# Kernel tuning notes

Hardware: AMD Instinct MI355X
Metric: run time of the kernel (lower is better)

## Reference

```python
import math
import jax, jax.numpy as jnp
import numpy as np

N_STEPS = 4
D_ENERGY = 128
FEATURE_DIM = 1024
B, N = 4, 2048


def setup_inputs() -> dict:
    key = jax.random.key(0)
    ks = jax.random.split(key, 5)
    scale = 1.0 / math.sqrt(FEATURE_DIM)
    return {
        "features": jax.random.normal(ks[0], (B, N, FEATURE_DIM), dtype=jnp.float32),
        "W_q": jax.random.normal(ks[1], (FEATURE_DIM, D_ENERGY), dtype=jnp.float32) * scale,
        "W_k": jax.random.normal(ks[2], (FEATURE_DIM, D_ENERGY), dtype=jnp.float32) * scale,
        "charge_w": jax.random.normal(ks[3], (FEATURE_DIM, 1), dtype=jnp.float32) * scale,
        "charge_b": jnp.zeros((1,), dtype=jnp.float32),
        "locality_scale": jnp.float32(1.0),
        "step_size": jnp.float32(0.5),
        "charge_decay": jnp.float32(0.3),
    }


def reference(features, W_q, W_k, charge_w, charge_b, locality_scale, step_size, charge_decay):
    Bn, Nn, _ = features.shape
    # compatibility: [B,N,N]
    Q = jnp.einsum("bnf,fe->bne", features, W_q)
    K = jnp.einsum("bnf,fe->bne", features, W_k)
    compat = jnp.einsum("bqe,bke->bqk", Q, K) / jnp.sqrt(jnp.float32(D_ENERGY))
    # locality bias: locality_scale / max(|i-j|, 1)
    pos = jnp.arange(Nn, dtype=jnp.float32)
    dist = jnp.maximum(jnp.abs(pos[None, :] - pos[:, None]), 1.0)
    locality = locality_scale / dist  # [N,N]
    # initial charge in (0,1): [B,N]
    charge = jax.nn.sigmoid(jnp.einsum("bnf,fo->bno", features, charge_w)[..., 0] + charge_b[0])
    base = compat + locality[None]  # [B,N,N], fixed across steps
    logits = base
    for _ in range(N_STEPS):
        attn = jax.nn.softmax(logits, axis=-1)
        received = attn.sum(axis=-2)  # [B,N] column sums
        charge = charge * (1.0 - charge_decay * jax.nn.sigmoid(received - 1.0))
        energy = -base * charge[..., :, None] * charge[..., None, :]
        logits = logits - step_size * energy
    return jax.nn.softmax(logits, axis=-1)
```

## Files before the change

kernel.cpp:

```cpp
#include <hip/hip_runtime.h>
#include <math.h>

namespace {
constexpr int NB = 4;
constexpr int NN = 2048;
constexpr int FD = 1024;
constexpr int DE = 128;
constexpr int BN = NB * NN;

constexpr size_t BASE_OFF  = 0;
constexpr size_t PARTQ_OFF = 0;
constexpr size_t PARTK_OFF = 4194304;
constexpr size_t FH_OFF    = 8388608;
constexpr size_t FL_OFF    = 12582912;
constexpr size_t QKHL_OFF  = 16777216;
constexpr size_t C_OFF     = QKHL_OFF + 2097152;
constexpr size_t R_OFF     = C_OFF + 5 * (size_t)BN;
}

typedef __attribute__((ext_vector_type(8))) short bf16x8;
typedef __attribute__((ext_vector_type(4))) float f32x4;

__device__ __forceinline__ unsigned short bf16_hi(float x) {
    unsigned u = __float_as_uint(x);
    unsigned r = (u + 0x7fffu + ((u >> 16) & 1u)) >> 16;
    return (unsigned short)r;
}
__device__ __forceinline__ float bf16_val(unsigned short h) {
    return __uint_as_float((unsigned)h << 16);
}


__global__ __launch_bounds__(256) void convert_F(
        const float* __restrict__ feat, unsigned short* __restrict__ Fh,
        unsigned short* __restrict__ Fl) {
    const int g = blockIdx.x * 256 + threadIdx.x;
    const int tile = g >> 6, lane = g & 63;
    const int tr = tile >> 5, fc = tile & 31;
    const int row = tr * 16 + (lane & 15);
    const int f0 = fc * 32 + (lane >> 4) * 8;
    const float* src = &feat[(size_t)row * FD + f0];
    ushort4 h0, l0, h1, l1;
    float4 a = *(const float4*)src;
    float4 b = *(const float4*)(src + 4);
    h0.x = bf16_hi(a.x); l0.x = bf16_hi(a.x - bf16_val(h0.x));
    h0.y = bf16_hi(a.y); l0.y = bf16_hi(a.y - bf16_val(h0.y));
    h0.z = bf16_hi(a.z); l0.z = bf16_hi(a.z - bf16_val(h0.z));
    h0.w = bf16_hi(a.w); l0.w = bf16_hi(a.w - bf16_val(h0.w));
    h1.x = bf16_hi(b.x); l1.x = bf16_hi(b.x - bf16_val(h1.x));
    h1.y = bf16_hi(b.y); l1.y = bf16_hi(b.y - bf16_val(h1.y));
    h1.z = bf16_hi(b.z); l1.z = bf16_hi(b.z - bf16_val(h1.z));
    h1.w = bf16_hi(b.w); l1.w = bf16_hi(b.w - bf16_val(h1.w));
    const size_t dst = (size_t)tile * 512 + lane * 8;
    *(ushort4*)&Fh[dst] = h0; *(ushort4*)&Fh[dst + 4] = h1;
    *(ushort4*)&Fl[dst] = l0; *(ushort4*)&Fl[dst + 4] = l1;
}

__global__ __launch_bounds__(256) void convert_W(
        const float* __restrict__ Wq, const float* __restrict__ Wk,
        unsigned short* __restrict__ Wqh, unsigned short* __restrict__ Wql,
        unsigned short* __restrict__ Wkh, unsigned short* __restrict__ Wkl) {
    const int g = blockIdx.x * 256 + threadIdx.x;
    const int tile = g >> 6, lane = g & 63;
    const int ec = tile >> 5, fc = tile & 31;
    const int e = ec * 16 + (lane & 15);
    const int f0 = fc * 32 + (lane >> 4) * 8;
    const float* W = blockIdx.y ? Wk : Wq;
    unsigned short* Th = blockIdx.y ? Wkh : Wqh;
    unsigned short* Tl = blockIdx.y ? Wkl : Wql;
    unsigned short hh[8], ll[8];
    #pragma unroll
    for (int j = 0; j < 8; ++j) {
        float v = W[(size_t)(f0 + j) * DE + e];
        hh[j] = bf16_hi(v); ll[j] = bf16_hi(v - bf16_val(hh[j]));
    }
    const size_t dst = (size_t)tile * 512 + lane * 8;
    *(ushort4*)&Th[dst]     = make_ushort4(hh[0], hh[1], hh[2], hh[3]);
    *(ushort4*)&Th[dst + 4] = make_ushort4(hh[4], hh[5], hh[6], hh[7]);
    *(ushort4*)&Tl[dst]     = make_ushort4(ll[0], ll[1], ll[2], ll[3]);
    *(ushort4*)&Tl[dst + 4] = make_ushort4(ll[4], ll[5], ll[6], ll[7]);
}

__global__ __launch_bounds__(256) void charge_init(
        const float* __restrict__ feat, const float* __restrict__ cw,
        const float* __restrict__ cb, float* __restrict__ c0,
        float* __restrict__ received) {
    const int wave = threadIdx.x >> 6, lane = threadIdx.x & 63;
    const int r = blockIdx.x * 4 + wave;
    const float* fr = feat + (size_t)r * FD;
    float s = 0.f;
    #pragma unroll
    for (int k = 0; k < 16; ++k) { int f = lane + 64 * k; s += fr[f] * cw[f]; }
    for (int off = 32; off > 0; off >>= 1) s += __shfl_xor(s, off);
    if (lane == 0) {
        float x = s + cb[0];
        c0[r] = 1.f / (1.f + __expf(-x));
        received[r] = 0.f;
    }
}

__global__ __launch_bounds__(256) void qk_mfma(
        const unsigned short* __restrict__ Fh, const unsigned short* __restrict__ Fl,
        const unsigned short* __restrict__ Wqh, const unsigned short* __restrict__ Wql,
        const unsigned short* __restrict__ Wkh, const unsigned short* __restrict__ Wkl,
        float* __restrict__ partQ, float* __restrict__ partK) {
    const int tid = threadIdx.x;
    const int w = tid >> 6, lane = tid & 63;
    const int quad = lane >> 4, l16 = lane & 15;
    const int kc = blockIdx.x;
    const int tr0 = blockIdx.y * 4;
    const unsigned short* Bh = (w < 2) ? Wqh : Wkh;
    const unsigned short* Bl = (w < 2) ? Wql : Wkl;
    const int ec0 = (w & 1) * 4;
    float* part = ((w < 2) ? partQ : partK) + (size_t)kc * BN * DE;

    f32x4 acc[4][4];
    #pragma unroll
    for (int a = 0; a < 4; ++a)
        #pragma unroll
        for (int c = 0; c < 4; ++c) acc[a][c] = (f32x4){0.f, 0.f, 0.f, 0.f};

    #pragma unroll 2
    for (int ch = 0; ch < 8; ++ch) {
        const int fc = kc * 8 + ch;
        bf16x8 aH[4], aL[4];
        #pragma unroll
        for (int rt = 0; rt < 4; ++rt) {
            const size_t off = ((size_t)((tr0 + rt) * 32 + fc) * 64 + lane) * 8;
            aH[rt] = *(const bf16x8*)&Fh[off];
            aL[rt] = *(const bf16x8*)&Fl[off];
        }
        #pragma unroll
        for (int ct = 0; ct < 4; ++ct) {
            const size_t off = ((size_t)((ec0 + ct) * 32 + fc) * 64 + lane) * 8;
            bf16x8 bH = *(const bf16x8*)&Bh[off];
            bf16x8 bL = *(const bf16x8*)&Bl[off];
            #pragma unroll
            for (int rt = 0; rt < 4; ++rt) {
                acc[rt][ct] = __builtin_amdgcn_mfma_f32_16x16x32_bf16(aH[rt], bH, acc[rt][ct], 0, 0, 0);
                acc[rt][ct] = __builtin_amdgcn_mfma_f32_16x16x32_bf16(aH[rt], bL, acc[rt][ct], 0, 0, 0);
                acc[rt][ct] = __builtin_amdgcn_mfma_f32_16x16x32_bf16(aL[rt], bH, acc[rt][ct], 0, 0, 0);
            }
        }
    }
    #pragma unroll
    for (int rt = 0; rt < 4; ++rt)
        #pragma unroll
        for (int ct = 0; ct < 4; ++ct)
            #pragma unroll
            for (int reg = 0; reg < 4; ++reg) {
                const int row = (tr0 + rt) * 16 + quad * 4 + reg;
                const int e = (ec0 + ct) * 16 + l16;
                part[(size_t)row * DE + e] = acc[rt][ct][reg];
            }
}

__global__ __launch_bounds__(256) void qk_reduce(
        const float* __restrict__ partQ, const float* __restrict__ partK,
        unsigned short* __restrict__ Qh, unsigned short* __restrict__ Ql,
        unsigned short* __restrict__ Kh, unsigned short* __restrict__ Kl) {
    const size_t i4 = ((size_t)blockIdx.x * 256 + threadIdx.x) * 4;
    float4 q = {0.f, 0.f, 0.f, 0.f}, k = {0.f, 0.f, 0.f, 0.f};
    #pragma unroll
    for (int c = 0; c < 4; ++c) {
        float4 a = *(const float4*)&partQ[(size_t)c * BN * DE + i4];
        float4 b = *(const float4*)&partK[(size_t)c * BN * DE + i4];
        q.x += a.x; q.y += a.y; q.z += a.z; q.w += a.w;
        k.x += b.x; k.y += b.y; k.z += b.z; k.w += b.w;
    }
    const int row = (int)(i4 >> 7);
    const int k0  = (int)(i4 & 127);
    const int kc = k0 >> 5, quad = (k0 >> 3) & 3, j = k0 & 7;
    const int lane = quad * 16 + (row & 15);
    const size_t dst = ((size_t)((row >> 4) * 4 + kc) * 64 + lane) * 8 + j;
    ushort4 h, l;
    h.x = bf16_hi(q.x); l.x = bf16_hi(q.x - bf16_val(h.x));
    h.y = bf16_hi(q.y); l.y = bf16_hi(q.y - bf16_val(h.y));
    h.z = bf16_hi(q.z); l.z = bf16_hi(q.z - bf16_val(h.z));
    h.w = bf16_hi(q.w); l.w = bf16_hi(q.w - bf16_val(h.w));
    *(ushort4*)&Qh[dst] = h; *(ushort4*)&Ql[dst] = l;
    h.x = bf16_hi(k.x); l.x = bf16_hi(k.x - bf16_val(h.x));
    h.y = bf16_hi(k.y); l.y = bf16_hi(k.y - bf16_val(h.y));
    h.z = bf16_hi(k.z); l.z = bf16_hi(k.z - bf16_val(h.z));
    h.w = bf16_hi(k.w); l.w = bf16_hi(k.w - bf16_val(h.w));
    *(ushort4*)&Kh[dst] = h; *(ushort4*)&Kl[dst] = l;
}

__global__ __launch_bounds__(256) void base_mfma(
        const unsigned short* __restrict__ Qh, const unsigned short* __restrict__ Ql,
        const unsigned short* __restrict__ Kh, const unsigned short* __restrict__ Kl,
        const float* __restrict__ d_ls, float* __restrict__ base) {
    const int tid = threadIdx.x;
    const int w = tid >> 6, lane = tid & 63;
    const int quad = lane >> 4, l16 = lane & 15;
    const int b = blockIdx.z;
    const int i0 = blockIdx.y * 128, j0 = blockIdx.x * 128;
    const int trA0 = (b * NN + i0) / 16 + w * 2;
    const int trB0 = (b * NN + j0) / 16;

    f32x4 acc[2][8];
    #pragma unroll
    for (int a = 0; a < 2; ++a)
        #pragma unroll
        for (int c = 0; c < 8; ++c) acc[a][c] = (f32x4){0.f, 0.f, 0.f, 0.f};

    #pragma unroll
    for (int kc = 0; kc < 4; ++kc) {
        bf16x8 aH[2], aL[2];
        #pragma unroll
        for (int rt = 0; rt < 2; ++rt) {
            const size_t off = ((size_t)((trA0 + rt) * 4 + kc) * 64 + lane) * 8;
            aH[rt] = *(const bf16x8*)&Qh[off];
            aL[rt] = *(const bf16x8*)&Ql[off];
        }
        #pragma unroll
        for (int ct = 0; ct < 8; ++ct) {
            const size_t off = ((size_t)((trB0 + ct) * 4 + kc) * 64 + lane) * 8;
            bf16x8 bH = *(const bf16x8*)&Kh[off];
            bf16x8 bL = *(const bf16x8*)&Kl[off];
            #pragma unroll
            for (int rt = 0; rt < 2; ++rt) {
                acc[rt][ct] = __builtin_amdgcn_mfma_f32_16x16x32_bf16(aH[rt], bH, acc[rt][ct], 0, 0, 0);
                acc[rt][ct] = __builtin_amdgcn_mfma_f32_16x16x32_bf16(aH[rt], bL, acc[rt][ct], 0, 0, 0);
                acc[rt][ct] = __builtin_amdgcn_mfma_f32_16x16x32_bf16(aL[rt], bH, acc[rt][ct], 0, 0, 0);
            }
        }
    }
    const float ls = d_ls[0];
    const float rs = 0.08838834764831845f;
    #pragma unroll
    for (int rt = 0; rt < 2; ++rt)
        #pragma unroll
        for (int reg = 0; reg < 4; ++reg) {
            const int i = i0 + w * 32 + rt * 16 + quad * 4 + reg;
            float* brow = base + ((size_t)b * NN + i) * NN;
            #pragma unroll
            for (int ct = 0; ct < 8; ++ct) {
                const int j = j0 + ct * 16 + l16;
                const float dist = fmaxf(fabsf((float)(i - j)), 1.0f);
                brow[j] = acc[rt][ct][reg] * rs + ls / dist;
            }
        }
}

template <bool WRITE_OUT>
__global__ __launch_bounds__(256) void step_pass(
        const float* __restrict__ base, const float* __restrict__ charge,
        const int t, const float* __restrict__ d_ss,
        float* __restrict__ received, float* __restrict__ out) {
    __shared__ float colsum[4][NN];
    const int tid = threadIdx.x;
    const int w = tid >> 6, lane = tid & 63;
    const int b = blockIdx.x >> 7;
    const int rbase = (blockIdx.x & 127) * 16;
    const float ss = d_ss[0];
    const size_t cb = (size_t)b << 11;

    float col_acc[32];
    #pragma unroll
    for (int q = 0; q < 32; ++q) col_acc[q] = 0.f;

    for (int rr = 0; rr < 4; ++rr) {
        const size_t ri = cb + rbase + w * 4 + rr;
        const float* row = base + ri * NN;
        float ci[4];
        for (int u = 0; u < t; ++u) ci[u] = charge[(size_t)(u + 1) * BN + ri] * ss;

        float x[32];
        float mx = -1e30f;
        #pragma unroll
        for (int k = 0; k < 8; ++k) {
            const int c = k * 256 + lane * 4;
            float4 bv = *(const float4*)&row[c];
            float m0 = 1.f, m1 = 1.f, m2 = 1.f, m3 = 1.f;
            for (int u = 0; u < t; ++u) {
                float4 cj = *(const float4*)&charge[(size_t)(u + 1) * BN + cb + c];
                m0 += ci[u] * cj.x; m1 += ci[u] * cj.y;
                m2 += ci[u] * cj.z; m3 += ci[u] * cj.w;
            }
            x[k * 4 + 0] = bv.x * m0; x[k * 4 + 1] = bv.y * m1;
            x[k * 4 + 2] = bv.z * m2; x[k * 4 + 3] = bv.w * m3;
            mx = fmaxf(mx, fmaxf(fmaxf(x[k * 4], x[k * 4 + 1]),
                                 fmaxf(x[k * 4 + 2], x[k * 4 + 3])));
        }
        #pragma unroll
        for (int off = 32; off > 0; off >>= 1) mx = fmaxf(mx, __shfl_xor(mx, off));

        float se = 0.f;
        #pragma unroll
        for (int q = 0; q < 32; ++q) { x[q] = __expf(x[q] - mx); se += x[q]; }
        #pragma unroll
        for (int off = 32; off > 0; off >>= 1) se += __shfl_xor(se, off);
        const float inv = 1.0f / se;

        if (WRITE_OUT) {
            #pragma unroll
            for (int k = 0; k < 8; ++k) {
                const int c = k * 256 + lane * 4;
                float4 o = {x[k * 4 + 0] * inv, x[k * 4 + 1] * inv,
                            x[k * 4 + 2] * inv, x[k * 4 + 3] * inv};
                *(float4*)&out[ri * NN + c] = o;
            }
        } else {
            #pragma unroll
            for (int q = 0; q < 32; ++q) col_acc[q] += x[q] * inv;
        }
    }

    if (!WRITE_OUT) {
        #pragma unroll
        for (int k = 0; k < 8; ++k) {
            const int c = k * 256 + lane * 4;
            *(float4*)&colsum[w][c] = *(float4*)&col_acc[k * 4];
        }
        __syncthreads();
        #pragma unroll
        for (int k = 0; k < 8; ++k) {
            const int c = tid + 256 * k;
            const float s = colsum[0][c] + colsum[1][c] + colsum[2][c] + colsum[3][c];
            atomicAdd(&received[cb + c], s);
        }
    }
}

__global__ __launch_bounds__(256) void charge_update(
        float* __restrict__ received, const float* __restrict__ d_decay,
        const float* __restrict__ c_prev, float* __restrict__ c_next) {
    const int r = blockIdx.x * 256 + threadIdx.x;
    const float recv = received[r];
    received[r] = 0.f;
    const float sg = 1.f / (1.f + __expf(1.f - recv));
    c_next[r] = c_prev[r] * (1.f - d_decay[0] * sg);
}

extern "C" void kernel_launch(void* const* d_in, const int* in_sizes, int n_in,
                              void* d_out, int out_size, void* d_ws, size_t ws_size,
                              hipStream_t stream) {
    const float* feat  = (const float*)d_in[0];
    const float* Wq    = (const float*)d_in[1];
    const float* Wk    = (const float*)d_in[2];
    const float* cw    = (const float*)d_in[3];
    const float* cb    = (const float*)d_in[4];
    const float* ls    = (const float*)d_in[5];
    const float* ssp   = (const float*)d_in[6];
    const float* decay = (const float*)d_in[7];

    float* ws   = (float*)d_ws;
    float* base = ws + BASE_OFF;
    float* partQ = ws + PARTQ_OFF;
    float* partK = ws + PARTK_OFF;
    unsigned short* Fh = (unsigned short*)(ws + FH_OFF);
    unsigned short* Fl = (unsigned short*)(ws + FL_OFF);
    unsigned short* qkhl = (unsigned short*)(ws + QKHL_OFF);
    unsigned short* Qh = qkhl;
    unsigned short* Ql = qkhl + (size_t)BN * DE;
    unsigned short* Kh = qkhl + (size_t)2 * BN * DE;
    unsigned short* Kl = qkhl + (size_t)3 * BN * DE;
    unsigned short* Wqh = qkhl;
    unsigned short* Wql = qkhl + (size_t)DE * FD;
    unsigned short* Wkh = qkhl + (size_t)2 * DE * FD;
    unsigned short* Wkl = qkhl + (size_t)3 * DE * FD;
    float* charge = ws + C_OFF;
    float* recv   = ws + R_OFF;
    float* out    = (float*)d_out;

    convert_F<<<BN * FD / 8 / 256, 256, 0, stream>>>(feat, Fh, Fl);
    convert_W<<<dim3(64, 2), 256, 0, stream>>>(Wq, Wk, Wqh, Wql, Wkh, Wkl);
    charge_init<<<BN / 4, 256, 0, stream>>>(feat, cw, cb, charge, recv);
    qk_mfma<<<dim3(4, BN / 64), 256, 0, stream>>>(Fh, Fl, Wqh, Wql, Wkh, Wkl, partQ, partK);
    qk_reduce<<<BN * DE / 4 / 256, 256, 0, stream>>>(partQ, partK, Qh, Ql, Kh, Kl);
    base_mfma<<<dim3(NN / 128, NN / 128, NB), 256, 0, stream>>>(Qh, Ql, Kh, Kl, ls, base);

    for (int t = 0; t < 4; ++t) {
        step_pass<false><<<BN / 16, 256, 0, stream>>>(base, charge, t, ssp, recv, nullptr);
        charge_update<<<BN / 256, 256, 0, stream>>>(
            recv, decay, charge + (size_t)t * BN, charge + (size_t)(t + 1) * BN);
    }
    step_pass<true><<<BN / 16, 256, 0, stream>>>(base, charge, 4, ssp, recv, out);
}
```

Measured before the change: 310.5 us.

## Process one row per wave in step pass and specialize step count at compile time

```diff
diff --git a/kernel.cpp b/kernel.cpp
--- a/kernel.cpp
+++ b/kernel.cpp
@@ -243,81 +243,89 @@
         }
 }
 
-template <bool WRITE_OUT>
+template <bool WRITE_OUT, int T>
 __global__ __launch_bounds__(256) void step_pass(
         const float* __restrict__ base, const float* __restrict__ charge,
-        const int t, const float* __restrict__ d_ss,
+        const float* __restrict__ d_ss,
         float* __restrict__ received, float* __restrict__ out) {
-    __shared__ float colsum[4][NN];
+    constexpr int CS_W = WRITE_OUT ? 1 : 2;
+    constexpr int CS_N = WRITE_OUT ? 1 : NN;
+    __shared__ float colsum[CS_W][CS_N];
     const int tid = threadIdx.x;
     const int w = tid >> 6, lane = tid & 63;
-    const int b = blockIdx.x >> 7;
-    const int rbase = (blockIdx.x & 127) * 16;
+    const int b = blockIdx.x >> 9;
+    const int rbase = (blockIdx.x & 511) * 4;
     const float ss = d_ss[0];
     const size_t cb = (size_t)b << 11;
-
-    float col_acc[32];
-    #pragma unroll
-    for (int q = 0; q < 32; ++q) col_acc[q] = 0.f;
-
-    for (int rr = 0; rr < 4; ++rr) {
-        const size_t ri = cb + rbase + w * 4 + rr;
-        const float* row = base + ri * NN;
-        float ci[4];
-        for (int u = 0; u < t; ++u) ci[u] = charge[(size_t)(u + 1) * BN + ri] * ss;
-
-        float x[32];
-        float mx = -1e30f;
+    const size_t ri = cb + rbase + w;
+    const float* row = base + ri * NN;
+
+    float ci[T > 0 ? T : 1];
+    #pragma unroll
+    for (int u = 0; u < T; ++u) ci[u] = charge[(size_t)(u + 1) * BN + ri] * ss;
+
+    float x[32];
+    float mx = -1e30f;
+    #pragma unroll
+    for (int k = 0; k < 8; ++k) {
+        const int c = k * 256 + lane * 4;
+        float4 bv = *(const float4*)&row[c];
+        float m0 = 1.f, m1 = 1.f, m2 = 1.f, m3 = 1.f;
+        #pragma unroll
+        for (int u = 0; u < T; ++u) {
+            float4 cj = *(const float4*)&charge[(size_t)(u + 1) * BN + cb + c];
+            m0 += ci[u] * cj.x; m1 += ci[u] * cj.y;
+            m2 += ci[u] * cj.z; m3 += ci[u] * cj.w;
+        }
+        x[k * 4 + 0] = bv.x * m0; x[k * 4 + 1] = bv.y * m1;
+        x[k * 4 + 2] = bv.z * m2; x[k * 4 + 3] = bv.w * m3;
+        mx = fmaxf(mx, fmaxf(fmaxf(x[k * 4], x[k * 4 + 1]),
+                             fmaxf(x[k * 4 + 2], x[k * 4 + 3])));
+    }
+    #pragma unroll
+    for (int off = 32; off > 0; off >>= 1) mx = fmaxf(mx, __shfl_xor(mx, off));
+
+    float se = 0.f;
+    #pragma unroll
+    for (int q = 0; q < 32; ++q) { x[q] = __expf(x[q] - mx); se += x[q]; }
+    #pragma unroll
+    for (int off = 32; off > 0; off >>= 1) se += __shfl_xor(se, off);
+    const float inv = 1.0f / se;
+
+    if (WRITE_OUT) {
         #pragma unroll
         for (int k = 0; k < 8; ++k) {
             const int c = k * 256 + lane * 4;
-            float4 bv = *(const float4*)&row[c];
-            float m0 = 1.f, m1 = 1.f, m2 = 1.f, m3 = 1.f;
-            for (int u = 0; u < t; ++u) {
-                float4 cj = *(const float4*)&charge[(size_t)(u + 1) * BN + cb + c];
-                m0 += ci[u] * cj.x; m1 += ci[u] * cj.y;
-                m2 += ci[u] * cj.z; m3 += ci[u] * cj.w;
-            }
-            x[k * 4 + 0] = bv.x * m0; x[k * 4 + 1] = bv.y * m1;
-            x[k * 4 + 2] = bv.z * m2; x[k * 4 + 3] = bv.w * m3;
-            mx = fmaxf(mx, fmaxf(fmaxf(x[k * 4], x[k * 4 + 1]),
-                                 fmaxf(x[k * 4 + 2], x[k * 4 + 3])));
-        }
-        #pragma unroll
-        for (int off = 32; off > 0; off >>= 1) mx = fmaxf(mx, __shfl_xor(mx, off));
-
-        float se = 0.f;
-        #pragma unroll
-        for (int q = 0; q < 32; ++q) { x[q] = __expf(x[q] - mx); se += x[q]; }
-        #pragma unroll
-        for (int off = 32; off > 0; off >>= 1) se += __shfl_xor(se, off);
-        const float inv = 1.0f / se;
-
-        if (WRITE_OUT) {
+            float4 o = {x[k * 4 + 0] * inv, x[k * 4 + 1] * inv,
+                        x[k * 4 + 2] * inv, x[k * 4 + 3] * inv};
+            *(float4*)&out[ri * NN + c] = o;
+        }
+    } else {
+        if (w < 2) {
             #pragma unroll
             for (int k = 0; k < 8; ++k) {
                 const int c = k * 256 + lane * 4;
                 float4 o = {x[k * 4 + 0] * inv, x[k * 4 + 1] * inv,
                             x[k * 4 + 2] * inv, x[k * 4 + 3] * inv};
-                *(float4*)&out[ri * NN + c] = o;
-            }
-        } else {
-            #pragma unroll
-            for (int q = 0; q < 32; ++q) col_acc[q] += x[q] * inv;
-        }
-    }
-
-    if (!WRITE_OUT) {
-        #pragma unroll
-        for (int k = 0; k < 8; ++k) {
-            const int c = k * 256 + lane * 4;
-            *(float4*)&colsum[w][c] = *(float4*)&col_acc[k * 4];
+                *(float4*)&colsum[w][c] = o;
+            }
+        }
+        __syncthreads();
+        if (w >= 2) {
+            #pragma unroll
+            for (int k = 0; k < 8; ++k) {
+                const int c = k * 256 + lane * 4;
+                float4 acc = *(const float4*)&colsum[w - 2][c];
+                acc.x += x[k * 4 + 0] * inv; acc.y += x[k * 4 + 1] * inv;
+                acc.z += x[k * 4 + 2] * inv; acc.w += x[k * 4 + 3] * inv;
+                *(float4*)&colsum[w - 2][c] = acc;
+            }
         }
         __syncthreads();
         #pragma unroll
         for (int k = 0; k < 8; ++k) {
             const int c = tid + 256 * k;
-            const float s = colsum[0][c] + colsum[1][c] + colsum[2][c] + colsum[3][c];
+            const float s = colsum[0][c] + colsum[1][c];
             atomicAdd(&received[cb + c], s);
         }
     }
@@ -371,10 +379,13 @@
     qk_reduce<<<BN * DE / 4 / 256, 256, 0, stream>>>(partQ, partK, Qh, Ql, Kh, Kl);
     base_mfma<<<dim3(NN / 128, NN / 128, NB), 256, 0, stream>>>(Qh, Ql, Kh, Kl, ls, base);
 
-    for (int t = 0; t < 4; ++t) {
-        step_pass<false><<<BN / 16, 256, 0, stream>>>(base, charge, t, ssp, recv, nullptr);
-        charge_update<<<BN / 256, 256, 0, stream>>>(
-            recv, decay, charge + (size_t)t * BN, charge + (size_t)(t + 1) * BN);
-    }
-    step_pass<true><<<BN / 16, 256, 0, stream>>>(base, charge, 4, ssp, recv, out);
-}
+    step_pass<false, 0><<<BN / 4, 256, 0, stream>>>(base, charge, ssp, recv, nullptr);
+    charge_update<<<BN / 256, 256, 0, stream>>>(recv, decay, charge, charge + (size_t)BN);
+    step_pass<false, 1><<<BN / 4, 256, 0, stream>>>(base, charge, ssp, recv, nullptr);
+    charge_update<<<BN / 256, 256, 0, stream>>>(recv, decay, charge + (size_t)BN, charge + (size_t)2 * BN);
+    step_pass<false, 2><<<BN / 4, 256, 0, stream>>>(base, charge, ssp, recv, nullptr);
+    charge_update<<<BN / 256, 256, 0, stream>>>(recv, decay, charge + (size_t)2 * BN, charge + (size_t)3 * BN);
+    step_pass<false, 3><<<BN / 4, 256, 0, stream>>>(base, charge, ssp, recv, nullptr);
+    charge_update<<<BN / 256, 256, 0, stream>>>(recv, decay, charge + (size_t)3 * BN, charge + (size_t)4 * BN);
+    step_pass<true, 4><<<BN / 4, 256, 0, stream>>>(base, charge, ssp, recv, out);
+}
```

New measurement: 331.7 us. 6.8% more time.

## Replace atomic column-sum accumulation with per-block partials and deterministic reduction

Applied to the files above, without the earlier changes.

```diff
diff --git a/kernel.cpp b/kernel.cpp
--- a/kernel.cpp
+++ b/kernel.cpp
@@ -15,7 +15,6 @@
 constexpr size_t FL_OFF    = 12582912;
 constexpr size_t QKHL_OFF  = 16777216;
 constexpr size_t C_OFF     = QKHL_OFF + 2097152;
-constexpr size_t R_OFF     = C_OFF + 5 * (size_t)BN;
 }
 
 typedef __attribute__((ext_vector_type(8))) short bf16x8;
@@ -83,8 +82,7 @@
 
 __global__ __launch_bounds__(256) void charge_init(
         const float* __restrict__ feat, const float* __restrict__ cw,
-        const float* __restrict__ cb, float* __restrict__ c0,
-        float* __restrict__ received) {
+        const float* __restrict__ cb, float* __restrict__ c0) {
     const int wave = threadIdx.x >> 6, lane = threadIdx.x & 63;
     const int r = blockIdx.x * 4 + wave;
     const float* fr = feat + (size_t)r * FD;
@@ -95,7 +93,6 @@
     if (lane == 0) {
         float x = s + cb[0];
         c0[r] = 1.f / (1.f + __expf(-x));
-        received[r] = 0.f;
     }
 }
 
@@ -243,28 +240,35 @@
         }
 }
 
-template <bool WRITE_OUT>
+template <int T, bool WO>
 __global__ __launch_bounds__(256) void step_pass(
         const float* __restrict__ base, const float* __restrict__ charge,
-        const int t, const float* __restrict__ d_ss,
-        float* __restrict__ received, float* __restrict__ out) {
-    __shared__ float colsum[4][NN];
+        const float* __restrict__ d_ss, float* __restrict__ P,
+        float* __restrict__ out) {
+    constexpr int CS_W = WO ? 1 : 4;
+    constexpr int CS_N = WO ? 1 : NN;
+    __shared__ float colsum[CS_W][CS_N];
     const int tid = threadIdx.x;
     const int w = tid >> 6, lane = tid & 63;
-    const int b = blockIdx.x >> 7;
-    const int rbase = (blockIdx.x & 127) * 16;
+    const int blk = blockIdx.x;
+    const int b = blk >> 8;
+    const int r0 = (blk & 255) * 8;
     const float ss = d_ss[0];
     const size_t cb = (size_t)b << 11;
 
     float col_acc[32];
-    #pragma unroll
-    for (int q = 0; q < 32; ++q) col_acc[q] = 0.f;
-
-    for (int rr = 0; rr < 4; ++rr) {
-        const size_t ri = cb + rbase + w * 4 + rr;
+    if (!WO) {
+        #pragma unroll
+        for (int q = 0; q < 32; ++q) col_acc[q] = 0.f;
+    }
+
+    #pragma unroll 1
+    for (int rr = 0; rr < 2; ++rr) {
+        const size_t ri = cb + r0 + w * 2 + rr;
         const float* row = base + ri * NN;
-        float ci[4];
-        for (int u = 0; u < t; ++u) ci[u] = charge[(size_t)(u + 1) * BN + ri] * ss;
+        float ci[T > 0 ? T : 1];
+        #pragma unroll
+        for (int u = 0; u < T; ++u) ci[u] = charge[(size_t)(u + 1) * BN + ri] * ss;
 
         float x[32];
         float mx = -1e30f;
@@ -273,7 +277,8 @@
             const int c = k * 256 + lane * 4;
             float4 bv = *(const float4*)&row[c];
             float m0 = 1.f, m1 = 1.f, m2 = 1.f, m3 = 1.f;
-            for (int u = 0; u < t; ++u) {
+            #pragma unroll
+            for (int u = 0; u < T; ++u) {
                 float4 cj = *(const float4*)&charge[(size_t)(u + 1) * BN + cb + c];
                 m0 += ci[u] * cj.x; m1 += ci[u] * cj.y;
                 m2 += ci[u] * cj.z; m3 += ci[u] * cj.w;
@@ -293,7 +298,7 @@
         for (int off = 32; off > 0; off >>= 1) se += __shfl_xor(se, off);
         const float inv = 1.0f / se;
 
-        if (WRITE_OUT) {
+        if (WO) {
             #pragma unroll
             for (int k = 0; k < 8; ++k) {
                 const int c = k * 256 + lane * 4;
@@ -307,30 +312,32 @@
         }
     }
 
-    if (!WRITE_OUT) {
-        #pragma unroll
-        for (int k = 0; k < 8; ++k) {
-            const int c = k * 256 + lane * 4;
-            *(float4*)&colsum[w][c] = *(float4*)&col_acc[k * 4];
-        }
+    if (!WO) {
+        #pragma unroll
+        for (int k = 0; k < 8; ++k)
+            *(float4*)&colsum[w][k * 256 + lane * 4] = *(float4*)&col_acc[k * 4];
         __syncthreads();
+        float* prow = P + (size_t)blk * NN;
         #pragma unroll
         for (int k = 0; k < 8; ++k) {
             const int c = tid + 256 * k;
-            const float s = colsum[0][c] + colsum[1][c] + colsum[2][c] + colsum[3][c];
-            atomicAdd(&received[cb + c], s);
-        }
-    }
-}
-
-__global__ __launch_bounds__(256) void charge_update(
-        float* __restrict__ received, const float* __restrict__ d_decay,
+            prow[c] = colsum[0][c] + colsum[1][c] + colsum[2][c] + colsum[3][c];
+        }
+    }
+}
+
+__global__ __launch_bounds__(256) void charge_reduce(
+        const float* __restrict__ P, const float* __restrict__ d_decay,
         const float* __restrict__ c_prev, float* __restrict__ c_next) {
-    const int r = blockIdx.x * 256 + threadIdx.x;
-    const float recv = received[r];
-    received[r] = 0.f;
-    const float sg = 1.f / (1.f + __expf(1.f - recv));
-    c_next[r] = c_prev[r] * (1.f - d_decay[0] * sg);
+    const int b = blockIdx.x >> 3;
+    const int col = ((blockIdx.x & 7) << 8) + threadIdx.x;
+    const float* p = P + ((size_t)b * 256) * NN + col;
+    float s = 0.f;
+    #pragma unroll 8
+    for (int r = 0; r < 256; ++r) s += p[(size_t)r * NN];
+    const int gi = (b << 11) + col;
+    const float sg = 1.f / (1.f + __expf(1.f - s));
+    c_next[gi] = c_prev[gi] * (1.f - d_decay[0] * sg);
 }
 
 extern "C" void kernel_launch(void* const* d_in, const int* in_sizes, int n_in,
@@ -361,20 +368,23 @@
     unsigned short* Wkh = qkhl + (size_t)2 * DE * FD;
     unsigned short* Wkl = qkhl + (size_t)3 * DE * FD;
     float* charge = ws + C_OFF;
-    float* recv   = ws + R_OFF;
+    float* P      = ws + QKHL_OFF;
     float* out    = (float*)d_out;
 
     convert_F<<<BN * FD / 8 / 256, 256, 0, stream>>>(feat, Fh, Fl);
     convert_W<<<dim3(64, 2), 256, 0, stream>>>(Wq, Wk, Wqh, Wql, Wkh, Wkl);
-    charge_init<<<BN / 4, 256, 0, stream>>>(feat, cw, cb, charge, recv);
+    charge_init<<<BN / 4, 256, 0, stream>>>(feat, cw, cb, charge);
     qk_mfma<<<dim3(4, BN / 64), 256, 0, stream>>>(Fh, Fl, Wqh, Wql, Wkh, Wkl, partQ, partK);
     qk_reduce<<<BN * DE / 4 / 256, 256, 0, stream>>>(partQ, partK, Qh, Ql, Kh, Kl);
     base_mfma<<<dim3(NN / 128, NN / 128, NB), 256, 0, stream>>>(Qh, Ql, Kh, Kl, ls, base);
 
-    for (int t = 0; t < 4; ++t) {
-        step_pass<false><<<BN / 16, 256, 0, stream>>>(base, charge, t, ssp, recv, nullptr);
-        charge_update<<<BN / 256, 256, 0, stream>>>(
-            recv, decay, charge + (size_t)t * BN, charge + (size_t)(t + 1) * BN);
-    }
-    step_pass<true><<<BN / 16, 256, 0, stream>>>(base, charge, 4, ssp, recv, out);
-}
+    step_pass<0, false><<<1024, 256, 0, stream>>>(base, charge, ssp, P, nullptr);
+    charge_reduce<<<32, 256, 0, stream>>>(P, decay, charge, charge + (size_t)BN);
+    step_pass<1, false><<<1024, 256, 0, stream>>>(base, charge, ssp, P, nullptr);
+    charge_reduce<<<32, 256, 0, stream>>>(P, decay, charge + (size_t)BN, charge + (size_t)2 * BN);
+    step_pass<2, false><<<1024, 256, 0, stream>>>(base, charge, ssp, P, nullptr);
+    charge_reduce<<<32, 256, 0, stream>>>(P, decay, charge + (size_t)2 * BN, charge + (size_t)3 * BN);
+    step_pass<3, false><<<1024, 256, 0, stream>>>(base, charge, ssp, P, nullptr);
+    charge_reduce<<<32, 256, 0, stream>>>(P, decay, charge + (size_t)3 * BN, charge + (size_t)4 * BN);
+    step_pass<4, true><<<1024, 256, 0, stream>>>(base, charge, ssp, nullptr, out);
+}
```

After: 299.7 us. 3.5% less time.
